# Performance work log

Measured on AMD Instinct MI355X. Metric: run time of the kernel, lower is better.

Reference implementation:

```python
import jax, jax.numpy as jnp
import numpy as np

NEG_SLOPE = 0.01  # nn.LeakyReLU default


def setup_inputs() -> dict:
    key = jax.random.key(0)
    ks = jax.random.split(key, 13)
    B, T, C = 128, 2048, 16
    CO = 8 * C          # 128 conv out channels == LSTM input
    H = 128             # LSTM hidden
    G = 4 * H           # gate dim
    OUT = 1
    s = 0.08            # keep recurrence stable over 2048 steps
    f32 = jnp.float32
    return {
        "x": jax.random.normal(ks[0], (B, T, C), f32),
        "conv_w": jax.random.normal(ks[1], (CO, C, 3), f32) * s,
        "conv_b": jax.random.normal(ks[2], (CO,), f32) * s,
        "w_ih0": jax.random.normal(ks[3], (G, CO), f32) * s,
        "w_hh0": jax.random.normal(ks[4], (G, H), f32) * s,
        "b_ih0": jax.random.normal(ks[5], (G,), f32) * s,
        "b_hh0": jax.random.normal(ks[6], (G,), f32) * s,
        "w_ih1": jax.random.normal(ks[7], (G, H), f32) * s,
        "w_hh1": jax.random.normal(ks[8], (G, H), f32) * s,
        "b_ih1": jax.random.normal(ks[9], (G,), f32) * s,
        "b_hh1": jax.random.normal(ks[10], (G,), f32) * s,
        "lin_w": jax.random.normal(ks[11], (OUT, H), f32) * s,
        "lin_b": jax.random.normal(ks[12], (OUT,), f32) * s,
    }


def _lstm_cell(gates, c):
    i, f, g, o = jnp.split(gates, 4, axis=-1)  # torch gate order i,f,g,o
    c_new = jax.nn.sigmoid(f) * c + jax.nn.sigmoid(i) * jnp.tanh(g)
    h_new = jax.nn.sigmoid(o) * jnp.tanh(c_new)
    return h_new, c_new


def reference(x, conv_w, conv_b, w_ih0, w_hh0, b_ih0, b_hh0,
              w_ih1, w_hh1, b_ih1, b_hh1, lin_w, lin_b):
    B, T, C = x.shape
    H = w_hh0.shape[1]
    # Conv1d k=3 pad=1 over time: [B,C,T] -> [B,8C,T]
    xc = jnp.transpose(x, (0, 2, 1))
    y = jax.lax.conv_general_dilated(
        xc, conv_w, window_strides=(1,), padding=((1, 1),),
        dimension_numbers=("NCH", "OIH", "NCH"))
    y = y + conv_b[None, :, None]
    y = jnp.where(y >= 0, y, NEG_SLOPE * y)  # LeakyReLU
    seq = jnp.transpose(y, (0, 2, 1))  # [B,T,8C]
    # Precompute layer-0 input projection (biases folded in, constant per step)
    x0 = jnp.einsum("btc,gc->btg", seq, w_ih0) + (b_ih0 + b_hh0)  # [B,T,4H]
    b1 = b_ih1 + b_hh1

    def step(carry, xt):
        h0, c0, h1, c1 = carry
        h0, c0 = _lstm_cell(xt + h0 @ w_hh0.T, c0)
        h1, c1 = _lstm_cell(h0 @ w_ih1.T + b1 + h1 @ w_hh1.T, c1)
        return (h0, c0, h1, c1), h1

    zeros = jnp.zeros((B, H), x.dtype)
    init = (zeros, zeros, zeros, zeros)
    xs = jnp.transpose(x0, (1, 0, 2))  # [T,B,4H]
    _, hs = jax.lax.scan(step, init, xs)  # [T,B,H]
    pooled = hs.mean(axis=0)  # adaptive_avg_pool1d(.,1) == mean over time
    return pooled @ lin_w.T + lin_b
```

## Files before the change

kernel.cpp:

```cpp
#include <hip/hip_runtime.h>
#include <hip/hip_fp16.h>
#include <cstdint>
#include <cstddef>

#define B_ 128
#define T_ 2048
#define C_ 16
#define CO_ 128
#define H_ 128
#define G_ 512
#define WCV 184
#define NBLK (72 + WCV)
#define L2E  1.4426950408889634f
#define L2E2 2.8853900817779268f

typedef _Float16 half8 __attribute__((ext_vector_type(8)));
typedef float f32x4 __attribute__((ext_vector_type(4)));

__device__ __forceinline__ unsigned packh2f(float a, float b) {
  union { _Float16 h[2]; unsigned u; } x;
  x.h[0] = (_Float16)a; x.h[1] = (_Float16)b;
  return x.u;
}

__device__ __forceinline__ float rcpf(float x) { return __builtin_amdgcn_rcpf(x); }

__device__ __forceinline__ float exp2f_(float x) {
#if __has_builtin(__builtin_amdgcn_exp2f)
  return __builtin_amdgcn_exp2f(x);
#else
  return __expf(x * 0.6931471805599453f);
#endif
}

__device__ __forceinline__ void block_sync() {
  asm volatile("s_waitcnt lgkmcnt(0)" ::: "memory");
  __builtin_amdgcn_s_barrier();
  asm volatile("" ::: "memory");
}

__device__ __forceinline__ int ld_rlx(const int* p) {
  return __hip_atomic_load(p, __ATOMIC_RELAXED, __HIP_MEMORY_SCOPE_AGENT);
}
__device__ __forceinline__ void st_rlx(int* p, int v) {
  __hip_atomic_store(p, v, __ATOMIC_RELAXED, __HIP_MEMORY_SCOPE_AGENT);
}

__device__ __forceinline__ float lstm_cell1(float iv, float fv, float gv,
                                            float ov, float& c) {
  gv = fminf(fmaxf(gv, -43.3f), 43.3f);
  float ei = exp2f_(-iv), ef = exp2f_(-fv), eg = exp2f_(gv);
  float P = (1.f + ei) * (eg + 1.f);
  float Q = 1.f + ef;
  float num = c * P + (eg - 1.f) * Q;
  float cN = num * rcpf(Q * P);
  c = cN;
  float cc = fminf(fmaxf(cN, -15.f), 15.f);
  float eo = exp2f_(-ov), ec = exp2f_(L2E2 * cc);
  return (ec - 1.f) * rcpf((1.f + eo) * (ec + 1.f));
}

__global__ __launch_bounds__(256) void pack_kernel(
    const float* __restrict__ w_ih0, const float* __restrict__ w_hh0,
    const float* __restrict__ w_ih1, const float* __restrict__ w_hh1,
    const float* __restrict__ b_ih1, const float* __restrict__ b_hh1,
    uint4* __restrict__ Wf0, uint4* __restrict__ Wih1f,
    uint4* __restrict__ Whh1f, uint4* __restrict__ WB0f,
    f32x4* __restrict__ b1fD) {
  int tid = blockIdx.x * 256 + threadIdx.x;
  if (tid < 24576) {
    int u = tid & 8191, L = u & 63, s = (u >> 6) & 3, tl = (u >> 8) & 3, w = u >> 10;
    int which = tid >> 13;
    const float* src = (which == 0) ? w_hh0 : (which == 1) ? w_ih1 : w_hh1;
    uint4* dst = (which == 0) ? Wf0 : (which == 1) ? Wih1f : Whh1f;
    int m = (w + 8 * tl) * 16 + (L & 15);
    float sc = (tl == 2) ? L2E2 : L2E;
    int k0 = s * 32 + (L >> 4) * 8;
    const float* p = src + m * 128 + k0;
    uint4 o;
    o.x = packh2f(p[0] * sc, p[1] * sc); o.y = packh2f(p[2] * sc, p[3] * sc);
    o.z = packh2f(p[4] * sc, p[5] * sc); o.w = packh2f(p[6] * sc, p[7] * sc);
    dst[u] = o;
  } else if (tid < 32768) {
    int u = tid - 24576, L = u & 63, s = (u >> 6) & 3, nt = u >> 8;
    int g = nt * 16 + (L & 15);
    float sc = ((nt >> 3) == 2) ? L2E2 : L2E;
    int k0 = s * 32 + (L >> 4) * 8;
    const float* p = w_ih0 + g * 128 + k0;
    uint4 o;
    o.x = packh2f(p[0] * sc, p[1] * sc); o.y = packh2f(p[2] * sc, p[3] * sc);
    o.z = packh2f(p[4] * sc, p[5] * sc); o.w = packh2f(p[6] * sc, p[7] * sc);
    WB0f[u] = o;
  } else if (tid < 34816) {
    int u2 = tid - 32768;
    int tl = u2 & 3, L = (u2 >> 2) & 63, w = u2 >> 8;
    int q = L >> 4;
    float sc = (tl == 2) ? L2E2 : L2E;
    f32x4 o;
#pragma unroll
    for (int reg = 0; reg < 4; ++reg) {
      int row = (w + 8 * tl) * 16 + q * 4 + reg;
      o[reg] = (b_ih1[row] + b_hh1[row]) * sc;
    }
    b1fD[u2] = o;
  }
}

__global__ __launch_bounds__(512, 1) void persist_kernel(
    const float* __restrict__ x, const float* __restrict__ conv_w,
    const float* __restrict__ conv_b, const float* __restrict__ b_ih0,
    const float* __restrict__ b_hh0,
    const uint4* __restrict__ Wf0, const uint4* __restrict__ Wih1f,
    const uint4* __restrict__ Whh1f, const uint4* __restrict__ WB0f,
    const f32x4* __restrict__ b1fD,
    uint4* __restrict__ x0f, uint2* __restrict__ h0g, uint4* __restrict__ z1f,
    float* __restrict__ psave, int* __restrict__ flags,
    int rmask, int rmask2) {
  __shared__ __align__(16) union {
    struct { float xs[34 * 16]; _Float16 yh[32 * 136]; _Float16 x0S[32 * 512]; } wk;
    struct { _Float16 h[2][16 * 136]; } rc;
    struct { _Float16 h4[2][576]; } rc4;
  } sm;

  int* xready = flags;
  int* l0p = flags + 2048;
  int* l0c = flags + 2560;
  int* z1p = flags + 3072;
  int* l1p = flags + 3200;

  const int bid = blockIdx.x;
  const int tid = threadIdx.x;
  const int w = tid >> 6, L = tid & 63, q = L >> 4, n = L & 15;

  if (bid < 32 || (bid >= 40 && bid < 72)) {
    const bool isL0 = bid < 32;
    const int rb = isL0 ? bid : bid - 40;
    const int grp = (rb & 7) * 4 + (rb >> 3);
    half8 WA[4][4];
    {
      const uint4* Wsrc = isL0 ? Wf0 : Whh1f;
#pragma unroll
      for (int tl = 0; tl < 4; ++tl)
#pragma unroll
        for (int s = 0; s < 4; ++s)
          WA[tl][s] = __builtin_bit_cast(half8, Wsrc[((w * 4 + tl) * 4 + s) * 64 + L]);
    }
    float cst = 0.f, pool = 0.f;
    for (int idx = tid; idx < 576; idx += 512) ((unsigned*)sm.rc4.h4)[idx] = 0u;
    __syncthreads();

    const int n4 = n & 3;
    const int n16 = (grp & 3) * 4 + n4;
    const int uc = w * 16 + (L >> 2);
    const int bc = L & 3;
    const int rsel = (L >> 2) & 3;
    const bool sb0 = (rsel & 1) != 0, sb1 = (rsel & 2) != 0;

    const uint4* rp = (isL0 ? x0f : z1f) +
        (((size_t)(grp >> 2) * 8 + w) * 64 + (q * 16 + n16)) * 2;
    const int rmk = isL0 ? rmask : rmask2;
    uint2* hgp = h0g + (((grp >> 2) * 16 + ((grp & 3) * 4 + (tid & 3))) * 32 + (tid >> 2));
    uint4 pa[4], pb[4];

    for (int g = 0; g < 64; ++g) {
      const int p0g = g * 32;
      if (tid == 0) {
        if (isL0) {
          while (ld_rlx(&xready[g * 32 + grp]) < 4) __builtin_amdgcn_s_sleep(2);
          if (g < 63)
            while (ld_rlx(&xready[(g + 1) * 32 + grp]) < 4) __builtin_amdgcn_s_sleep(2);
        } else {
          int tgt = p0g + 40; if (tgt > T_) tgt = T_;
          while (ld_rlx(&z1p[(grp >> 2) * 16]) < tgt) __builtin_amdgcn_s_sleep(1);
        }
        __builtin_amdgcn_fence(__ATOMIC_ACQUIRE, "agent");
      }
      block_sync();
      if (g == 0) {
#pragma unroll
        for (int k = 0; k < 4; ++k) {
          pa[k] = rp[(size_t)k * 8192];
          pb[k] = rp[(size_t)k * 8192 + 1];
        }
      }
#pragma unroll 1
      for (int io = 0; io < 8; ++io) {
#pragma unroll
        for (int k = 0; k < 4; ++k) {
          const int t = p0g + io * 4 + k;
          const int c = t & 1, p = c ^ 1;
          f32x4 acc[4];
          {
            half8 xlo = __builtin_bit_cast(half8, pa[k]);
            half8 xhi = __builtin_bit_cast(half8, pb[k]);
            acc[0] = (f32x4){(float)xlo[0], (float)xlo[1], (float)xlo[2], (float)xlo[3]};
            acc[1] = (f32x4){(float)xlo[4], (float)xlo[5], (float)xlo[6], (float)xlo[7]};
            acc[2] = (f32x4){(float)xhi[0], (float)xhi[1], (float)xhi[2], (float)xhi[3]};
            acc[3] = (f32x4){(float)xhi[4], (float)xhi[5], (float)xhi[6], (float)xhi[7]};
          }
          half8 B0[4];
#pragma unroll
          for (int s = 0; s < 4; ++s)
            B0[s] = *(const half8*)&sm.rc4.h4[p][n4 * 144 + s * 32 + q * 8];
#pragma unroll
          for (int s = 0; s < 4; ++s)
#pragma unroll
            for (int tl = 0; tl < 4; ++tl)
              acc[tl] = __builtin_amdgcn_mfma_f32_16x16x32_f16(WA[tl][s], B0[s], acc[tl], 0, 0, 0);

          {
            int tn = t + 4; if (tn > T_ - 1) tn = T_ - 1;
            const size_t so = (size_t)(tn & rmk) * 8192;
            pa[k] = rp[so];
            pb[k] = rp[so + 1];
          }

          float gi, gf, gg, go;
          {
            float lo, hi;
            lo = sb0 ? acc[0][1] : acc[0][0]; hi = sb0 ? acc[0][3] : acc[0][2];
            gi = sb1 ? hi : lo;
            lo = sb0 ? acc[1][1] : acc[1][0]; hi = sb0 ? acc[1][3] : acc[1][2];
            gf = sb1 ? hi : lo;
            lo = sb0 ? acc[2][1] : acc[2][0]; hi = sb0 ? acc[2][3] : acc[2][2];
            gg = sb1 ? hi : lo;
            lo = sb0 ? acc[3][1] : acc[3][0]; hi = sb0 ? acc[3][3] : acc[3][2];
            go = sb1 ? hi : lo;
          }
          float hv = lstm_cell1(gi, gf, gg, go, cst);
          if (!isL0) pool += hv;
          sm.rc4.h4[c][bc * 144 + uc] = (_Float16)hv;

          block_sync();
          if (isL0) {
            if (k == 3) {
              asm volatile("s_waitcnt vmcnt(8)" ::: "memory");
              if (tid == 0) st_rlx(&l0p[grp * 16], t - 3);
            }
            if (tid < 128)
              hgp[(size_t)t * 4096] =
                  *(const uint2*)&sm.rc4.h4[c][(tid & 3) * 144 + (tid >> 2) * 4];
          }
        }
      }
      if (tid == 0) {
        if (isL0) st_rlx(&l0c[grp * 16], p0g + 32);
        else if (g & 1) st_rlx(&l1p[grp * 16], p0g + 32);
      }
    }
    if (isL0) {
      asm volatile("s_waitcnt vmcnt(0)" ::: "memory");
      __builtin_amdgcn_s_barrier();
      if (tid == 0)
        __hip_atomic_store(&l0p[grp * 16], T_, __ATOMIC_RELEASE,
                           __HIP_MEMORY_SCOPE_AGENT);
    } else {
      psave[(size_t)(grp * 4 + bc) * 128 + uc] = pool;
    }
  } else if (bid < 40) {
    const int b16 = bid - 32;
    half8 WI[4][4];
#pragma unroll
    for (int tl = 0; tl < 4; ++tl)
#pragma unroll
      for (int s = 0; s < 4; ++s)
        WI[tl][s] = __builtin_bit_cast(half8, Wih1f[((w * 4 + tl) * 4 + s) * 64 + L]);
    f32x4 b1v[4];
#pragma unroll
    for (int tl = 0; tl < 4; ++tl) b1v[tl] = b1fD[(w * 64 + L) * 4 + tl];

    const int n2 = tid >> 5, jq = tid & 31;
    const uint2* hsrc = h0g + ((b16 * 16 + n2) * 32 + jq);
    uint4* zdst = z1f + (((size_t)b16 * 8 + w) * 64 + L) * 2;
    const int R2 = rmask2 + 1;
    uint2 hpf[4];

#pragma unroll 1
    for (int p0 = 0; p0 < T_; p0 += 4) {
      if (tid < 4) {
        const int gj = b16 * 4 + tid;
        while (ld_rlx(&l0p[gj * 16]) < p0 + 4) __builtin_amdgcn_s_sleep(1);
        __builtin_amdgcn_fence(__ATOMIC_ACQUIRE, "agent");
      } else if (tid >= 4 && tid < 8 && p0 + 4 > R2) {
        const int gj = b16 * 4 + (tid - 4);
        const int need = p0 + 12 - R2;
        while (ld_rlx(&l1p[gj * 16]) < need) __builtin_amdgcn_s_sleep(8);
      }
      block_sync();
#pragma unroll
      for (int k = 0; k < 4; ++k) hpf[k] = hsrc[(size_t)(p0 + k) * 4096];
#pragma unroll
      for (int k = 0; k < 4; ++k) {
        const int t = p0 + k;
        const int c = t & 1;
        *(uint2*)&sm.rc.h[c][n2 * 136 + jq * 4] = hpf[k];
        block_sync();
        half8 B[4];
#pragma unroll
        for (int s = 0; s < 4; ++s)
          B[s] = *(const half8*)&sm.rc.h[c][n * 136 + s * 32 + q * 8];
        f32x4 acc[4];
#pragma unroll
        for (int tl = 0; tl < 4; ++tl) acc[tl] = b1v[tl];
#pragma unroll
        for (int s = 0; s < 4; ++s)
#pragma unroll
          for (int tl = 0; tl < 4; ++tl)
            acc[tl] = __builtin_amdgcn_mfma_f32_16x16x32_f16(WI[tl][s], B[s], acc[tl], 0, 0, 0);
        uint4 o0, o1;
        o0.x = packh2f(acc[0][0], acc[0][1]); o0.y = packh2f(acc[0][2], acc[0][3]);
        o0.z = packh2f(acc[1][0], acc[1][1]); o0.w = packh2f(acc[1][2], acc[1][3]);
        o1.x = packh2f(acc[2][0], acc[2][1]); o1.y = packh2f(acc[2][2], acc[2][3]);
        o1.z = packh2f(acc[3][0], acc[3][1]); o1.w = packh2f(acc[3][2], acc[3][3]);
        const size_t zs = (size_t)(t & rmask2) * 8192;
        zdst[zs] = o0;
        zdst[zs + 1] = o1;
      }
      asm volatile("s_waitcnt vmcnt(12)" ::: "memory");
      block_sync();
      if (tid == 0) st_rlx(&z1p[b16 * 16], p0);
    }
    asm volatile("s_waitcnt vmcnt(0)" ::: "memory");
    __builtin_amdgcn_s_barrier();
    if (tid == 0)
      __hip_atomic_store(&z1p[b16 * 16], T_, __ATOMIC_RELEASE,
                         __HIP_MEMORY_SCOPE_AGENT);
  } else {
    const int wi = bid - 72;
    const int co = tid & 127;
    float cw[48];
#pragma unroll
    for (int i = 0; i < 12; ++i) {
      const float4 v = *(const float4*)(conv_w + co * 48 + i * 4);
      cw[i * 4 + 0] = v.x; cw[i * 4 + 1] = v.y;
      cw[i * 4 + 2] = v.z; cw[i * 4 + 3] = v.w;
    }
    const float cb = conv_b[co];
    half8 WB[4][4];
#pragma unroll
    for (int nt4 = 0; nt4 < 4; ++nt4)
#pragma unroll
      for (int s = 0; s < 4; ++s)
        WB[nt4][s] = __builtin_bit_cast(half8, WB0f[((w * 4 + nt4) * 4 + s) * 64 + L]);
    float b0v[4];
#pragma unroll
    for (int nt4 = 0; nt4 < 4; ++nt4) {
      int gg = (w * 4 + nt4) * 16 + n;
      b0v[nt4] = (b_ih0[gg] + b_hh0[gg]) * (((gg >> 7) == 2) ? L2E2 : L2E);
    }
    const int R = rmask + 1;

    for (int u = wi; u < 8192; u += WCV) {
      const int tile = u >> 7, b = u & 127;
      const int t0c = tile * 32;
      if (t0c + 40 > R) {
        const int need = t0c + 40 - R;
        if (tid == 0)
          while (ld_rlx(&l0c[(b >> 2) * 16]) < need)
            __builtin_amdgcn_s_sleep(8);
      }
      __syncthreads();

      for (int idx = tid; idx < 544; idx += 512) {
        int row = idx >> 4, cc2 = idx & 15;
        int gt = t0c - 1 + row;
        sm.wk.xs[idx] = (gt >= 0 && gt < T_) ? x[((size_t)b * T_ + gt) * C_ + cc2] : 0.f;
      }
      __syncthreads();

#pragma unroll
      for (int pp = 0; pp < 8; ++pp) {
        int r = pp * 4 + (tid >> 7);
        float acc = cb;
#pragma unroll
        for (int c16 = 0; c16 < 16; ++c16)
#pragma unroll
          for (int kk = 0; kk < 3; ++kk)
            acc += sm.wk.xs[(r + kk) * 16 + c16] * cw[c16 * 3 + kk];
        acc = acc >= 0.f ? acc : 0.01f * acc;
        sm.wk.yh[r * 136 + co] = (_Float16)acc;
      }
      __syncthreads();

#pragma unroll
      for (int mt = 0; mt < 2; ++mt) {
        half8 A[4];
#pragma unroll
        for (int s = 0; s < 4; ++s)
          A[s] = *(const half8*)&sm.wk.yh[(mt * 16 + n) * 136 + s * 32 + q * 8];
#pragma unroll
        for (int nt4 = 0; nt4 < 4; ++nt4) {
          f32x4 acc = {b0v[nt4], b0v[nt4], b0v[nt4], b0v[nt4]};
#pragma unroll
          for (int s = 0; s < 4; ++s)
            acc = __builtin_amdgcn_mfma_f32_16x16x32_f16(A[s], WB[nt4][s], acc, 0, 0, 0);
          int tau = w * 4 + nt4;
          int off = (tau & 7) * 64 + (n >> 2) * 16 + (tau >> 3) * 4 + (n & 3);
#pragma unroll
          for (int reg = 0; reg < 4; ++reg)
            sm.wk.x0S[(mt * 16 + q * 4 + reg) * 512 + off] = (_Float16)acc[reg];
        }
      }
      __syncthreads();

      const int bn = b & 15, bb16 = b >> 4;
      const int trb = t0c & rmask;
#pragma unroll
      for (int kk = 0; kk < 2; ++kk) {
        int cc = kk * 512 + tid;
        int r = cc >> 5, wq = cc & 31;
        int w2 = wq >> 2, q2 = wq & 3;
        const uint4* src = (const uint4*)&sm.wk.x0S[r * 512 + wq * 16];
        size_t gidx = ((((size_t)(trb + r) * 8 + bb16) * 8 + w2) * 64 + (bn + 16 * q2)) * 2;
        x0f[gidx] = src[0];
        x0f[gidx + 1] = src[1];
      }
      asm volatile("s_waitcnt vmcnt(0)" ::: "memory");
      __syncthreads();
      if (tid == 0)
        __hip_atomic_fetch_add(&xready[tile * 32 + (b >> 2)], 1, __ATOMIC_RELEASE,
                               __HIP_MEMORY_SCOPE_AGENT);
    }
  }
}

__global__ __launch_bounds__(128) void final_kernel(
    const float* __restrict__ psave, const float* __restrict__ lin_w,
    const float* __restrict__ lin_b, float* __restrict__ out) {
  int b = threadIdx.x;
  float acc = 0.f;
  const f32x4* pv = (const f32x4*)(psave + (size_t)b * 128);
  const f32x4* lw = (const f32x4*)lin_w;
#pragma unroll
  for (int u = 0; u < 32; ++u) {
    f32x4 v = pv[u], l = lw[u];
    acc += v[0] * l[0] + v[1] * l[1] + v[2] * l[2] + v[3] * l[3];
  }
  out[b] = acc * (1.0f / (float)T_) + lin_b[0];
}

extern "C" void kernel_launch(void* const* d_in, const int* in_sizes, int n_in,
                              void* d_out, int out_size, void* d_ws, size_t ws_size,
                              hipStream_t stream) {
  (void)in_sizes; (void)n_in; (void)out_size;
  const float* x      = (const float*)d_in[0];
  const float* conv_w = (const float*)d_in[1];
  const float* conv_b = (const float*)d_in[2];
  const float* w_ih0  = (const float*)d_in[3];
  const float* w_hh0  = (const float*)d_in[4];
  const float* b_ih0  = (const float*)d_in[5];
  const float* b_hh0  = (const float*)d_in[6];
  const float* w_ih1  = (const float*)d_in[7];
  const float* w_hh1  = (const float*)d_in[8];
  const float* b_ih1  = (const float*)d_in[9];
  const float* b_hh1  = (const float*)d_in[10];
  const float* lin_w  = (const float*)d_in[11];
  const float* lin_b  = (const float*)d_in[12];

  char* ws = (char*)d_ws;
  uint4* Wf0   = (uint4*)(ws + 0);
  uint4* Wih1f = (uint4*)(ws + 131072);
  uint4* Whh1f = (uint4*)(ws + 262144);
  uint4* WB0f  = (uint4*)(ws + 393216);
  f32x4* b1fD  = (f32x4*)(ws + 524288);
  float* psave = (float*)(ws + 557056);
  int*   flags = (int*)(ws + 622592);
  uint2* h0g   = (uint2*)(ws + 638976);
  const size_t base = 638976 + 67108864;

  int R = 256, R2 = 256;
  while (R > 64 && base + ((size_t)R + (size_t)R2) * 131072 > ws_size) {
    R >>= 1; R2 >>= 1;
  }
  uint4* x0f = (uint4*)(ws + base);
  uint4* z1f = (uint4*)(ws + base + (size_t)R * 131072);

  hipMemsetAsync(flags, 0, 16384, stream);
  pack_kernel<<<136, 256, 0, stream>>>(w_ih0, w_hh0, w_ih1, w_hh1, b_ih1, b_hh1,
                                       Wf0, Wih1f, Whh1f, WB0f, b1fD);
  persist_kernel<<<NBLK, 512, 0, stream>>>(
      x, conv_w, conv_b, b_ih0, b_hh0, Wf0, Wih1f, Whh1f, WB0f, b1fD,
      x0f, h0g, z1f, psave, flags, R - 1, R2 - 1);
  final_kernel<<<1, 128, 0, stream>>>(psave, lin_w, lin_b, (float*)d_out);
}
```

Before: 1.643 ms.

## Fuse layer-1 input projection into layer-1 recurrent blocks, drop z1 stage

Removes the 8 dedicated blocks that computed the layer-1 input projection (h0 @ W_ih1 + b1) into a global z1 ring buffer. Each layer-1 recurrent block now reads h0 from global into shared memory with a short prefetch and does both the W_ih1 and W_hh1 MFMAs per step. The conv/projection blocks grow from 184 to 192 to use the freed slots. This cuts a pipeline stage, its flags and its global round-trips, but doubles the MFMA work and register weight footprint on the layer-1 critical path.

Measured after the change: 1.637 ms. Within noise of the previous version (-0.3%).

```diff
diff --git a/kernel.cpp b/kernel.cpp
--- a/kernel.cpp
+++ b/kernel.cpp
@@ -9,8 +9,8 @@
 #define CO_ 128
 #define H_ 128
 #define G_ 512
-#define WCV 184
-#define NBLK (72 + WCV)
+#define WCV 192
+#define NBLK (64 + WCV)
 #define L2E  1.4426950408889634f
 #define L2E2 2.8853900817779268f
 
@@ -113,40 +113,31 @@
     const uint4* __restrict__ Wf0, const uint4* __restrict__ Wih1f,
     const uint4* __restrict__ Whh1f, const uint4* __restrict__ WB0f,
     const f32x4* __restrict__ b1fD,
-    uint4* __restrict__ x0f, uint2* __restrict__ h0g, uint4* __restrict__ z1f,
-    float* __restrict__ psave, int* __restrict__ flags,
-    int rmask, int rmask2) {
+    uint4* __restrict__ x0f, uint2* __restrict__ h0g,
+    float* __restrict__ psave, int* __restrict__ flags, int rmask) {
   __shared__ __align__(16) union {
     struct { float xs[34 * 16]; _Float16 yh[32 * 136]; _Float16 x0S[32 * 512]; } wk;
-    struct { _Float16 h[2][16 * 136]; } rc;
-    struct { _Float16 h4[2][576]; } rc4;
+    struct { _Float16 hb[2][576]; _Float16 h0b[2][576]; } rc4;
   } sm;
 
   int* xready = flags;
-  int* l0p = flags + 2048;
-  int* l0c = flags + 2560;
-  int* z1p = flags + 3072;
-  int* l1p = flags + 3200;
+  int* l0c = flags + 2048;
+  int* l0p = flags + 2560;
 
   const int bid = blockIdx.x;
   const int tid = threadIdx.x;
   const int w = tid >> 6, L = tid & 63, q = L >> 4, n = L & 15;
 
-  if (bid < 32 || (bid >= 40 && bid < 72)) {
-    const bool isL0 = bid < 32;
-    const int rb = isL0 ? bid : bid - 40;
-    const int grp = (rb & 7) * 4 + (rb >> 3);
+  if (bid < 32) {
+    const int grp = (bid & 7) * 4 + (bid >> 3);
     half8 WA[4][4];
-    {
-      const uint4* Wsrc = isL0 ? Wf0 : Whh1f;
-#pragma unroll
-      for (int tl = 0; tl < 4; ++tl)
-#pragma unroll
-        for (int s = 0; s < 4; ++s)
-          WA[tl][s] = __builtin_bit_cast(half8, Wsrc[((w * 4 + tl) * 4 + s) * 64 + L]);
-    }
-    float cst = 0.f, pool = 0.f;
-    for (int idx = tid; idx < 576; idx += 512) ((unsigned*)sm.rc4.h4)[idx] = 0u;
+#pragma unroll
+    for (int tl = 0; tl < 4; ++tl)
+#pragma unroll
+      for (int s = 0; s < 4; ++s)
+        WA[tl][s] = __builtin_bit_cast(half8, Wf0[((w * 4 + tl) * 4 + s) * 64 + L]);
+    float cst = 0.f;
+    for (int idx = tid; idx < 576; idx += 512) ((unsigned*)sm.rc4.hb)[idx] = 0u;
     __syncthreads();
 
     const int n4 = n & 3;
@@ -156,23 +147,16 @@
     const int rsel = (L >> 2) & 3;
     const bool sb0 = (rsel & 1) != 0, sb1 = (rsel & 2) != 0;
 
-    const uint4* rp = (isL0 ? x0f : z1f) +
-        (((size_t)(grp >> 2) * 8 + w) * 64 + (q * 16 + n16)) * 2;
-    const int rmk = isL0 ? rmask : rmask2;
+    const uint4* rp = x0f + (((size_t)(grp >> 2) * 8 + w) * 64 + (q * 16 + n16)) * 2;
     uint2* hgp = h0g + (((grp >> 2) * 16 + ((grp & 3) * 4 + (tid & 3))) * 32 + (tid >> 2));
     uint4 pa[4], pb[4];
 
     for (int g = 0; g < 64; ++g) {
       const int p0g = g * 32;
       if (tid == 0) {
-        if (isL0) {
-          while (ld_rlx(&xready[g * 32 + grp]) < 4) __builtin_amdgcn_s_sleep(2);
-          if (g < 63)
-            while (ld_rlx(&xready[(g + 1) * 32 + grp]) < 4) __builtin_amdgcn_s_sleep(2);
-        } else {
-          int tgt = p0g + 40; if (tgt > T_) tgt = T_;
-          while (ld_rlx(&z1p[(grp >> 2) * 16]) < tgt) __builtin_amdgcn_s_sleep(1);
-        }
+        while (ld_rlx(&xready[g * 32 + grp]) < 4) __builtin_amdgcn_s_sleep(2);
+        if (g < 63)
+          while (ld_rlx(&xready[(g + 1) * 32 + grp]) < 4) __builtin_amdgcn_s_sleep(2);
         __builtin_amdgcn_fence(__ATOMIC_ACQUIRE, "agent");
       }
       block_sync();
@@ -201,7 +185,7 @@
           half8 B0[4];
 #pragma unroll
           for (int s = 0; s < 4; ++s)
-            B0[s] = *(const half8*)&sm.rc4.h4[p][n4 * 144 + s * 32 + q * 8];
+            B0[s] = *(const half8*)&sm.rc4.hb[p][n4 * 144 + s * 32 + q * 8];
 #pragma unroll
           for (int s = 0; s < 4; ++s)
 #pragma unroll
@@ -210,7 +194,7 @@
 
           {
             int tn = t + 4; if (tn > T_ - 1) tn = T_ - 1;
-            const size_t so = (size_t)(tn & rmk) * 8192;
+            const size_t so = (size_t)(tn & rmask) * 8192;
             pa[k] = rp[so];
             pb[k] = rp[so + 1];
           }
@@ -228,105 +212,129 @@
             go = sb1 ? hi : lo;
           }
           float hv = lstm_cell1(gi, gf, gg, go, cst);
-          if (!isL0) pool += hv;
-          sm.rc4.h4[c][bc * 144 + uc] = (_Float16)hv;
+          sm.rc4.hb[c][bc * 144 + uc] = (_Float16)hv;
 
           block_sync();
-          if (isL0) {
-            if (k == 3) {
-              asm volatile("s_waitcnt vmcnt(8)" ::: "memory");
-              if (tid == 0) st_rlx(&l0p[grp * 16], t - 3);
-            }
-            if (tid < 128)
-              hgp[(size_t)t * 4096] =
-                  *(const uint2*)&sm.rc4.h4[c][(tid & 3) * 144 + (tid >> 2) * 4];
-          }
+          if (k == 3) {
+            asm volatile("s_waitcnt vmcnt(8)" ::: "memory");
+            if (tid == 0) st_rlx(&l0p[grp * 16], t - 3);
+          }
+          if (tid < 128)
+            hgp[(size_t)t * 4096] =
+                *(const uint2*)&sm.rc4.hb[c][(tid & 3) * 144 + (tid >> 2) * 4];
         }
       }
-      if (tid == 0) {
-        if (isL0) st_rlx(&l0c[grp * 16], p0g + 32);
-        else if (g & 1) st_rlx(&l1p[grp * 16], p0g + 32);
-      }
-    }
-    if (isL0) {
-      asm volatile("s_waitcnt vmcnt(0)" ::: "memory");
-      __builtin_amdgcn_s_barrier();
-      if (tid == 0)
-        __hip_atomic_store(&l0p[grp * 16], T_, __ATOMIC_RELEASE,
-                           __HIP_MEMORY_SCOPE_AGENT);
-    } else {
-      psave[(size_t)(grp * 4 + bc) * 128 + uc] = pool;
-    }
-  } else if (bid < 40) {
-    const int b16 = bid - 32;
-    half8 WI[4][4];
-#pragma unroll
-    for (int tl = 0; tl < 4; ++tl)
-#pragma unroll
-      for (int s = 0; s < 4; ++s)
-        WI[tl][s] = __builtin_bit_cast(half8, Wih1f[((w * 4 + tl) * 4 + s) * 64 + L]);
-    f32x4 b1v[4];
-#pragma unroll
-    for (int tl = 0; tl < 4; ++tl) b1v[tl] = b1fD[(w * 64 + L) * 4 + tl];
-
-    const int n2 = tid >> 5, jq = tid & 31;
-    const uint2* hsrc = h0g + ((b16 * 16 + n2) * 32 + jq);
-    uint4* zdst = z1f + (((size_t)b16 * 8 + w) * 64 + L) * 2;
-    const int R2 = rmask2 + 1;
-    uint2 hpf[4];
-
-#pragma unroll 1
-    for (int p0 = 0; p0 < T_; p0 += 4) {
-      if (tid < 4) {
-        const int gj = b16 * 4 + tid;
-        while (ld_rlx(&l0p[gj * 16]) < p0 + 4) __builtin_amdgcn_s_sleep(1);
-        __builtin_amdgcn_fence(__ATOMIC_ACQUIRE, "agent");
-      } else if (tid >= 4 && tid < 8 && p0 + 4 > R2) {
-        const int gj = b16 * 4 + (tid - 4);
-        const int need = p0 + 12 - R2;
-        while (ld_rlx(&l1p[gj * 16]) < need) __builtin_amdgcn_s_sleep(8);
-      }
-      block_sync();
-#pragma unroll
-      for (int k = 0; k < 4; ++k) hpf[k] = hsrc[(size_t)(p0 + k) * 4096];
-#pragma unroll
-      for (int k = 0; k < 4; ++k) {
-        const int t = p0 + k;
-        const int c = t & 1;
-        *(uint2*)&sm.rc.h[c][n2 * 136 + jq * 4] = hpf[k];
-        block_sync();
-        half8 B[4];
-#pragma unroll
-        for (int s = 0; s < 4; ++s)
-          B[s] = *(const half8*)&sm.rc.h[c][n * 136 + s * 32 + q * 8];
-        f32x4 acc[4];
-#pragma unroll
-        for (int tl = 0; tl < 4; ++tl) acc[tl] = b1v[tl];
-#pragma unroll
-        for (int s = 0; s < 4; ++s)
-#pragma unroll
-          for (int tl = 0; tl < 4; ++tl)
-            acc[tl] = __builtin_amdgcn_mfma_f32_16x16x32_f16(WI[tl][s], B[s], acc[tl], 0, 0, 0);
-        uint4 o0, o1;
-        o0.x = packh2f(acc[0][0], acc[0][1]); o0.y = packh2f(acc[0][2], acc[0][3]);
-        o0.z = packh2f(acc[1][0], acc[1][1]); o0.w = packh2f(acc[1][2], acc[1][3]);
-        o1.x = packh2f(acc[2][0], acc[2][1]); o1.y = packh2f(acc[2][2], acc[2][3]);
-        o1.z = packh2f(acc[3][0], acc[3][1]); o1.w = packh2f(acc[3][2], acc[3][3]);
-        const size_t zs = (size_t)(t & rmask2) * 8192;
-        zdst[zs] = o0;
-        zdst[zs + 1] = o1;
-      }
-      asm volatile("s_waitcnt vmcnt(12)" ::: "memory");
-      block_sync();
-      if (tid == 0) st_rlx(&z1p[b16 * 16], p0);
+      if (tid == 0) st_rlx(&l0c[grp * 16], p0g + 32);
     }
     asm volatile("s_waitcnt vmcnt(0)" ::: "memory");
     __builtin_amdgcn_s_barrier();
     if (tid == 0)
-      __hip_atomic_store(&z1p[b16 * 16], T_, __ATOMIC_RELEASE,
+      __hip_atomic_store(&l0p[grp * 16], T_, __ATOMIC_RELEASE,
                          __HIP_MEMORY_SCOPE_AGENT);
+  } else if (bid < 64) {
+    const int rb = bid - 32;
+    const int grp = (rb & 7) * 4 + (rb >> 3);
+    half8 WA[4][4], WI[4][4];
+#pragma unroll
+    for (int tl = 0; tl < 4; ++tl)
+#pragma unroll
+      for (int s = 0; s < 4; ++s) {
+        WA[tl][s] = __builtin_bit_cast(half8, Whh1f[((w * 4 + tl) * 4 + s) * 64 + L]);
+        WI[tl][s] = __builtin_bit_cast(half8, Wih1f[((w * 4 + tl) * 4 + s) * 64 + L]);
+      }
+    f32x4 b1v[4];
+#pragma unroll
+    for (int tl = 0; tl < 4; ++tl) b1v[tl] = b1fD[(w * 64 + L) * 4 + tl];
+
+    float cst = 0.f, pool = 0.f;
+    for (int idx = tid; idx < 1152; idx += 512) ((unsigned*)&sm.rc4)[idx] = 0u;
+    __syncthreads();
+
+    const int n4 = n & 3;
+    const int uc = w * 16 + (L >> 2);
+    const int bc = L & 3;
+    const int rsel = (L >> 2) & 3;
+    const bool sb0 = (rsel & 1) != 0, sb1 = (rsel & 2) != 0;
+
+    const uint2* hgp = h0g + (((size_t)(grp >> 2) * 16 + ((grp & 3) * 4 + (tid & 3))) * 32 + (tid >> 2));
+    const int h0off = (tid & 3) * 144 + (tid >> 2) * 4;
+    uint2 pf[4];
+
+    if (tid == 0) {
+      while (ld_rlx(&l0p[grp * 16]) < 8) __builtin_amdgcn_s_sleep(1);
+      __builtin_amdgcn_fence(__ATOMIC_ACQUIRE, "agent");
+    }
+    block_sync();
+    if (tid < 128) {
+      uint2 h00 = hgp[0];
+      *(uint2*)&sm.rc4.h0b[0][h0off] = h00;
+#pragma unroll
+      for (int k = 0; k < 4; ++k) pf[k] = hgp[(size_t)(k + 1) * 4096];
+    }
+    block_sync();
+
+#pragma unroll 1
+    for (int g = 0; g < 64; ++g) {
+      const int p0g = g * 32;
+      if (tid == 0) {
+        int tgt = p0g + 40; if (tgt > T_) tgt = T_;
+        while (ld_rlx(&l0p[grp * 16]) < tgt) __builtin_amdgcn_s_sleep(1);
+        __builtin_amdgcn_fence(__ATOMIC_ACQUIRE, "agent");
+      }
+      block_sync();
+#pragma unroll 1
+      for (int io = 0; io < 8; ++io) {
+#pragma unroll
+        for (int k = 0; k < 4; ++k) {
+          const int t = p0g + io * 4 + k;
+          const int c = t & 1, p = c ^ 1;
+          half8 B1[4], B0h[4];
+#pragma unroll
+          for (int s = 0; s < 4; ++s) {
+            B1[s] = *(const half8*)&sm.rc4.hb[p][n4 * 144 + s * 32 + q * 8];
+            B0h[s] = *(const half8*)&sm.rc4.h0b[c][n4 * 144 + s * 32 + q * 8];
+          }
+          if (tid < 128) {
+            *(uint2*)&sm.rc4.h0b[p][h0off] = pf[k];
+            int tn = t + 5; if (tn > T_ - 1) tn = T_ - 1;
+            pf[k] = hgp[(size_t)tn * 4096];
+          }
+          f32x4 acc[4];
+#pragma unroll
+          for (int tl = 0; tl < 4; ++tl) acc[tl] = b1v[tl];
+#pragma unroll
+          for (int s = 0; s < 4; ++s)
+#pragma unroll
+            for (int tl = 0; tl < 4; ++tl)
+              acc[tl] = __builtin_amdgcn_mfma_f32_16x16x32_f16(WI[tl][s], B0h[s], acc[tl], 0, 0, 0);
+#pragma unroll
+          for (int s = 0; s < 4; ++s)
+#pragma unroll
+            for (int tl = 0; tl < 4; ++tl)
+              acc[tl] = __builtin_amdgcn_mfma_f32_16x16x32_f16(WA[tl][s], B1[s], acc[tl], 0, 0, 0);
+
+          float gi, gf, gg, go;
+          {
+            float lo, hi;
+            lo = sb0 ? acc[0][1] : acc[0][0]; hi = sb0 ? acc[0][3] : acc[0][2];
+            gi = sb1 ? hi : lo;
+            lo = sb0 ? acc[1][1] : acc[1][0]; hi = sb0 ? acc[1][3] : acc[1][2];
+            gf = sb1 ? hi : lo;
+            lo = sb0 ? acc[2][1] : acc[2][0]; hi = sb0 ? acc[2][3] : acc[2][2];
+            gg = sb1 ? hi : lo;
+            lo = sb0 ? acc[3][1] : acc[3][0]; hi = sb0 ? acc[3][3] : acc[3][2];
+            go = sb1 ? hi : lo;
+          }
+          float hv = lstm_cell1(gi, gf, gg, go, cst);
+          pool += hv;
+          sm.rc4.hb[c][bc * 144 + uc] = (_Float16)hv;
+          block_sync();
+        }
+      }
+    }
+    psave[(size_t)(grp * 4 + bc) * 128 + uc] = pool;
   } else {
-    const int wi = bid - 72;
+    const int wi = bid - 64;
     const int co = tid & 127;
     float cw[48];
 #pragma unroll
@@ -468,18 +476,15 @@
   uint2* h0g   = (uint2*)(ws + 638976);
   const size_t base = 638976 + 67108864;
 
-  int R = 256, R2 = 256;
-  while (R > 64 && base + ((size_t)R + (size_t)R2) * 131072 > ws_size) {
-    R >>= 1; R2 >>= 1;
-  }
+  int R = 256;
+  while (R > 64 && base + (size_t)R * 131072 > ws_size) R >>= 1;
   uint4* x0f = (uint4*)(ws + base);
-  uint4* z1f = (uint4*)(ws + base + (size_t)R * 131072);
 
   hipMemsetAsync(flags, 0, 16384, stream);
   pack_kernel<<<136, 256, 0, stream>>>(w_ih0, w_hh0, w_ih1, w_hh1, b_ih1, b_hh1,
                                        Wf0, Wih1f, Whh1f, WB0f, b1fD);
   persist_kernel<<<NBLK, 512, 0, stream>>>(
       x, conv_w, conv_b, b_ih0, b_hh0, Wf0, Wih1f, Whh1f, WB0f, b1fD,
-      x0f, h0g, z1f, psave, flags, R - 1, R2 - 1);
+      x0f, h0g, psave, flags, R - 1);
   final_kernel<<<1, 128, 0, stream>>>(psave, lin_w, lin_b, (float*)d_out);
 }
```

## Merge layer-0 and layer-1 recurrence blocks into skewed single blocks

Applied to the files above, without the earlier changes.

The separate layer-0 and layer-1 recurrent block sets are merged, so each of 32 blocks now runs both recurrences. Layer 1 trails layer 0 by a fixed lag of 56 steps and shares the per-step barrier, with a tail loop that finishes the last lagged steps. This frees 32 blocks, which go to the conv/input-projection workers (WCV 184 to 216). The cost is more work per step on the critical serial path, more registers for both weight sets, and tighter coupling to the z1 producer through the lag.

Measured after the change: 2.308 ms. 1.4x slower.

```diff
diff --git a/kernel.cpp b/kernel.cpp
--- a/kernel.cpp
+++ b/kernel.cpp
@@ -9,8 +9,9 @@
 #define CO_ 128
 #define H_ 128
 #define G_ 512
-#define WCV 184
-#define NBLK (72 + WCV)
+#define LAG 56
+#define WCV 216
+#define NBLK (40 + WCV)
 #define L2E  1.4426950408889634f
 #define L2E2 2.8853900817779268f
 
@@ -58,6 +59,12 @@
   float cc = fminf(fmaxf(cN, -15.f), 15.f);
   float eo = exp2f_(-ov), ec = exp2f_(L2E2 * cc);
   return (ec - 1.f) * rcpf((1.f + eo) * (ec + 1.f));
+}
+
+__device__ __forceinline__ float sel4(const f32x4 v, bool sb0, bool sb1) {
+  float lo = sb0 ? v[1] : v[0];
+  float hi = sb0 ? v[3] : v[2];
+  return sb1 ? hi : lo;
 }
 
 __global__ __launch_bounds__(256) void pack_kernel(
@@ -119,7 +126,7 @@
   __shared__ __align__(16) union {
     struct { float xs[34 * 16]; _Float16 yh[32 * 136]; _Float16 x0S[32 * 512]; } wk;
     struct { _Float16 h[2][16 * 136]; } rc;
-    struct { _Float16 h4[2][576]; } rc4;
+    struct { _Float16 h0b[2][576]; _Float16 h1b[2][576]; } rcm;
   } sm;
 
   int* xready = flags;
@@ -132,23 +139,8 @@
   const int tid = threadIdx.x;
   const int w = tid >> 6, L = tid & 63, q = L >> 4, n = L & 15;
 
-  if (bid < 32 || (bid >= 40 && bid < 72)) {
-    const bool isL0 = bid < 32;
-    const int rb = isL0 ? bid : bid - 40;
-    const int grp = (rb & 7) * 4 + (rb >> 3);
-    half8 WA[4][4];
-    {
-      const uint4* Wsrc = isL0 ? Wf0 : Whh1f;
-#pragma unroll
-      for (int tl = 0; tl < 4; ++tl)
-#pragma unroll
-        for (int s = 0; s < 4; ++s)
-          WA[tl][s] = __builtin_bit_cast(half8, Wsrc[((w * 4 + tl) * 4 + s) * 64 + L]);
-    }
-    float cst = 0.f, pool = 0.f;
-    for (int idx = tid; idx < 576; idx += 512) ((unsigned*)sm.rc4.h4)[idx] = 0u;
-    __syncthreads();
-
+  if (bid < 32) {
+    const int grp = (bid & 7) * 4 + (bid >> 3);
     const int n4 = n & 3;
     const int n16 = (grp & 3) * 4 + n4;
     const int uc = w * 16 + (L >> 2);
@@ -156,107 +148,171 @@
     const int rsel = (L >> 2) & 3;
     const bool sb0 = (rsel & 1) != 0, sb1 = (rsel & 2) != 0;
 
-    const uint4* rp = (isL0 ? x0f : z1f) +
-        (((size_t)(grp >> 2) * 8 + w) * 64 + (q * 16 + n16)) * 2;
-    const int rmk = isL0 ? rmask : rmask2;
+    half8 WA0[4][4], WA1[4][4];
+#pragma unroll
+    for (int tl = 0; tl < 4; ++tl)
+#pragma unroll
+      for (int s = 0; s < 4; ++s) {
+        WA0[tl][s] = __builtin_bit_cast(half8, Wf0[((w * 4 + tl) * 4 + s) * 64 + L]);
+        WA1[tl][s] = __builtin_bit_cast(half8, Whh1f[((w * 4 + tl) * 4 + s) * 64 + L]);
+      }
+
+    float c0 = 0.f, c1 = 0.f, pool = 0.f;
+    for (int idx = tid; idx < 1152; idx += 512) ((unsigned*)&sm.rcm)[idx] = 0u;
+    __syncthreads();
+
+    const uint4* rp = x0f + (((size_t)(grp >> 2) * 8 + w) * 64 + (q * 16 + n16)) * 2;
+    const uint4* zp = z1f + (((size_t)(grp >> 2) * 8 + w) * 64 + (q * 16 + n16)) * 2;
     uint2* hgp = h0g + (((grp >> 2) * 16 + ((grp & 3) * 4 + (tid & 3))) * 32 + (tid >> 2));
-    uint4 pa[4], pb[4];
+    uint4 pa, pb, za, zb;
 
     for (int g = 0; g < 64; ++g) {
       const int p0g = g * 32;
       if (tid == 0) {
-        if (isL0) {
-          while (ld_rlx(&xready[g * 32 + grp]) < 4) __builtin_amdgcn_s_sleep(2);
-          if (g < 63)
-            while (ld_rlx(&xready[(g + 1) * 32 + grp]) < 4) __builtin_amdgcn_s_sleep(2);
-        } else {
-          int tgt = p0g + 40; if (tgt > T_) tgt = T_;
-          while (ld_rlx(&z1p[(grp >> 2) * 16]) < tgt) __builtin_amdgcn_s_sleep(1);
-        }
+        while (ld_rlx(&xready[g * 32 + grp]) < 4) __builtin_amdgcn_s_sleep(2);
+        if (g < 63)
+          while (ld_rlx(&xready[(g + 1) * 32 + grp]) < 4) __builtin_amdgcn_s_sleep(2);
+        const int zt = p0g - 16;
+        if (zt > 0)
+          while (ld_rlx(&z1p[(grp >> 2) * 16]) < zt) __builtin_amdgcn_s_sleep(1);
         __builtin_amdgcn_fence(__ATOMIC_ACQUIRE, "agent");
       }
       block_sync();
-      if (g == 0) {
-#pragma unroll
-        for (int k = 0; k < 4; ++k) {
-          pa[k] = rp[(size_t)k * 8192];
-          pb[k] = rp[(size_t)k * 8192 + 1];
-        }
-      }
+      if (g == 0) { pa = rp[0]; pb = rp[1]; }
+      if (g == 1) { za = zp[0]; zb = zp[1]; }
 #pragma unroll 1
       for (int io = 0; io < 8; ++io) {
 #pragma unroll
         for (int k = 0; k < 4; ++k) {
           const int t = p0g + io * 4 + k;
-          const int c = t & 1, p = c ^ 1;
-          f32x4 acc[4];
+          const int u = t - LAG;
+          const int ct = t & 1, pt = ct ^ 1;
+
           {
-            half8 xlo = __builtin_bit_cast(half8, pa[k]);
-            half8 xhi = __builtin_bit_cast(half8, pb[k]);
-            acc[0] = (f32x4){(float)xlo[0], (float)xlo[1], (float)xlo[2], (float)xlo[3]};
-            acc[1] = (f32x4){(float)xlo[4], (float)xlo[5], (float)xlo[6], (float)xlo[7]};
-            acc[2] = (f32x4){(float)xhi[0], (float)xhi[1], (float)xhi[2], (float)xhi[3]};
-            acc[3] = (f32x4){(float)xhi[4], (float)xhi[5], (float)xhi[6], (float)xhi[7]};
+            half8 B0[4];
+#pragma unroll
+            for (int s = 0; s < 4; ++s)
+              B0[s] = *(const half8*)&sm.rcm.h0b[pt][n4 * 144 + s * 32 + q * 8];
+            f32x4 acc[4];
+            {
+              half8 xlo = __builtin_bit_cast(half8, pa);
+              half8 xhi = __builtin_bit_cast(half8, pb);
+              acc[0] = (f32x4){(float)xlo[0], (float)xlo[1], (float)xlo[2], (float)xlo[3]};
+              acc[1] = (f32x4){(float)xlo[4], (float)xlo[5], (float)xlo[6], (float)xlo[7]};
+              acc[2] = (f32x4){(float)xhi[0], (float)xhi[1], (float)xhi[2], (float)xhi[3]};
+              acc[3] = (f32x4){(float)xhi[4], (float)xhi[5], (float)xhi[6], (float)xhi[7]};
+            }
+            {
+              int tn = t + 1; if (tn > T_ - 1) tn = T_ - 1;
+              const size_t so = (size_t)(tn & rmask) * 8192;
+              pa = rp[so];
+              pb = rp[so + 1];
+            }
+#pragma unroll
+            for (int s = 0; s < 4; ++s)
+#pragma unroll
+              for (int tl = 0; tl < 4; ++tl)
+                acc[tl] = __builtin_amdgcn_mfma_f32_16x16x32_f16(WA0[tl][s], B0[s], acc[tl], 0, 0, 0);
+            float gi = sel4(acc[0], sb0, sb1);
+            float gf = sel4(acc[1], sb0, sb1);
+            float gg = sel4(acc[2], sb0, sb1);
+            float go = sel4(acc[3], sb0, sb1);
+            float hv = lstm_cell1(gi, gf, gg, go, c0);
+            sm.rcm.h0b[ct][bc * 144 + uc] = (_Float16)hv;
           }
-          half8 B0[4];
-#pragma unroll
-          for (int s = 0; s < 4; ++s)
-            B0[s] = *(const half8*)&sm.rc4.h4[p][n4 * 144 + s * 32 + q * 8];
-#pragma unroll
-          for (int s = 0; s < 4; ++s)
-#pragma unroll
-            for (int tl = 0; tl < 4; ++tl)
-              acc[tl] = __builtin_amdgcn_mfma_f32_16x16x32_f16(WA[tl][s], B0[s], acc[tl], 0, 0, 0);
-
-          {
-            int tn = t + 4; if (tn > T_ - 1) tn = T_ - 1;
-            const size_t so = (size_t)(tn & rmk) * 8192;
-            pa[k] = rp[so];
-            pb[k] = rp[so + 1];
+
+          if (u >= 0) {
+            half8 B1[4];
+#pragma unroll
+            for (int s = 0; s < 4; ++s)
+              B1[s] = *(const half8*)&sm.rcm.h1b[pt][n4 * 144 + s * 32 + q * 8];
+            f32x4 acc[4];
+            {
+              half8 xlo = __builtin_bit_cast(half8, za);
+              half8 xhi = __builtin_bit_cast(half8, zb);
+              acc[0] = (f32x4){(float)xlo[0], (float)xlo[1], (float)xlo[2], (float)xlo[3]};
+              acc[1] = (f32x4){(float)xlo[4], (float)xlo[5], (float)xlo[6], (float)xlo[7]};
+              acc[2] = (f32x4){(float)xhi[0], (float)xhi[1], (float)xhi[2], (float)xhi[3]};
+              acc[3] = (f32x4){(float)xhi[4], (float)xhi[5], (float)xhi[6], (float)xhi[7]};
+            }
+            {
+              const size_t so = (size_t)((u + 1) & rmask2) * 8192;
+              za = zp[so];
+              zb = zp[so + 1];
+            }
+#pragma unroll
+            for (int s = 0; s < 4; ++s)
+#pragma unroll
+              for (int tl = 0; tl < 4; ++tl)
+                acc[tl] = __builtin_amdgcn_mfma_f32_16x16x32_f16(WA1[tl][s], B1[s], acc[tl], 0, 0, 0);
+            float gi = sel4(acc[0], sb0, sb1);
+            float gf = sel4(acc[1], sb0, sb1);
+            float gg = sel4(acc[2], sb0, sb1);
+            float go = sel4(acc[3], sb0, sb1);
+            float hv = lstm_cell1(gi, gf, gg, go, c1);
+            pool += hv;
+            sm.rcm.h1b[ct][bc * 144 + uc] = (_Float16)hv;
           }
 
-          float gi, gf, gg, go;
-          {
-            float lo, hi;
-            lo = sb0 ? acc[0][1] : acc[0][0]; hi = sb0 ? acc[0][3] : acc[0][2];
-            gi = sb1 ? hi : lo;
-            lo = sb0 ? acc[1][1] : acc[1][0]; hi = sb0 ? acc[1][3] : acc[1][2];
-            gf = sb1 ? hi : lo;
-            lo = sb0 ? acc[2][1] : acc[2][0]; hi = sb0 ? acc[2][3] : acc[2][2];
-            gg = sb1 ? hi : lo;
-            lo = sb0 ? acc[3][1] : acc[3][0]; hi = sb0 ? acc[3][3] : acc[3][2];
-            go = sb1 ? hi : lo;
+          block_sync();
+          if (k == 3) {
+            asm volatile("s_waitcnt vmcnt(12)" ::: "memory");
+            if (tid == 0) st_rlx(&l0p[grp * 16], t - 3);
           }
-          float hv = lstm_cell1(gi, gf, gg, go, cst);
-          if (!isL0) pool += hv;
-          sm.rc4.h4[c][bc * 144 + uc] = (_Float16)hv;
-
-          block_sync();
-          if (isL0) {
-            if (k == 3) {
-              asm volatile("s_waitcnt vmcnt(8)" ::: "memory");
-              if (tid == 0) st_rlx(&l0p[grp * 16], t - 3);
-            }
-            if (tid < 128)
-              hgp[(size_t)t * 4096] =
-                  *(const uint2*)&sm.rc4.h4[c][(tid & 3) * 144 + (tid >> 2) * 4];
-          }
+          if (tid < 128)
+            hgp[(size_t)t * 4096] =
+                *(const uint2*)&sm.rcm.h0b[ct][(tid & 3) * 144 + (tid >> 2) * 4];
         }
       }
       if (tid == 0) {
-        if (isL0) st_rlx(&l0c[grp * 16], p0g + 32);
-        else if (g & 1) st_rlx(&l1p[grp * 16], p0g + 32);
-      }
-    }
-    if (isL0) {
-      asm volatile("s_waitcnt vmcnt(0)" ::: "memory");
-      __builtin_amdgcn_s_barrier();
-      if (tid == 0)
-        __hip_atomic_store(&l0p[grp * 16], T_, __ATOMIC_RELEASE,
-                           __HIP_MEMORY_SCOPE_AGENT);
-    } else {
-      psave[(size_t)(grp * 4 + bc) * 128 + uc] = pool;
-    }
+        st_rlx(&l0c[grp * 16], p0g + 32);
+        const int lp = p0g - 24;
+        if (lp > 0) st_rlx(&l1p[grp * 16], lp);
+      }
+    }
+    asm volatile("s_waitcnt vmcnt(0)" ::: "memory");
+    __builtin_amdgcn_s_barrier();
+    if (tid == 0)
+      __hip_atomic_store(&l0p[grp * 16], T_, __ATOMIC_RELEASE,
+                         __HIP_MEMORY_SCOPE_AGENT);
+#pragma unroll 1
+    for (int u = T_ - LAG; u < T_; ++u) {
+      if (tid == 0) {
+        while (ld_rlx(&z1p[(grp >> 2) * 16]) < u + 1) __builtin_amdgcn_s_sleep(1);
+        __builtin_amdgcn_fence(__ATOMIC_ACQUIRE, "agent");
+      }
+      block_sync();
+      const int cu = u & 1, pu = cu ^ 1;
+      half8 B1[4];
+#pragma unroll
+      for (int s = 0; s < 4; ++s)
+        B1[s] = *(const half8*)&sm.rcm.h1b[pu][n4 * 144 + s * 32 + q * 8];
+      const size_t zs = (size_t)(u & rmask2) * 8192;
+      uint4 za2 = zp[zs], zb2 = zp[zs + 1];
+      f32x4 acc[4];
+      {
+        half8 xlo = __builtin_bit_cast(half8, za2);
+        half8 xhi = __builtin_bit_cast(half8, zb2);
+        acc[0] = (f32x4){(float)xlo[0], (float)xlo[1], (float)xlo[2], (float)xlo[3]};
+        acc[1] = (f32x4){(float)xlo[4], (float)xlo[5], (float)xlo[6], (float)xlo[7]};
+        acc[2] = (f32x4){(float)xhi[0], (float)xhi[1], (float)xhi[2], (float)xhi[3]};
+        acc[3] = (f32x4){(float)xhi[4], (float)xhi[5], (float)xhi[6], (float)xhi[7]};
+      }
+#pragma unroll
+      for (int s = 0; s < 4; ++s)
+#pragma unroll
+        for (int tl = 0; tl < 4; ++tl)
+          acc[tl] = __builtin_amdgcn_mfma_f32_16x16x32_f16(WA1[tl][s], B1[s], acc[tl], 0, 0, 0);
+      float gi = sel4(acc[0], sb0, sb1);
+      float gf = sel4(acc[1], sb0, sb1);
+      float gg = sel4(acc[2], sb0, sb1);
+      float go = sel4(acc[3], sb0, sb1);
+      float hv = lstm_cell1(gi, gf, gg, go, c1);
+      pool += hv;
+      sm.rcm.h1b[cu][bc * 144 + uc] = (_Float16)hv;
+      block_sync();
+    }
+    psave[(size_t)(grp * 4 + bc) * 128 + uc] = pool;
   } else if (bid < 40) {
     const int b16 = bid - 32;
     half8 WI[4][4];
@@ -326,7 +382,7 @@
       __hip_atomic_store(&z1p[b16 * 16], T_, __ATOMIC_RELEASE,
                          __HIP_MEMORY_SCOPE_AGENT);
   } else {
-    const int wi = bid - 72;
+    const int wi = bid - 40;
     const int co = tid & 127;
     float cw[48];
 #pragma unroll
@@ -425,11 +481,11 @@
 }
 
 __global__ __launch_bounds__(128) void final_kernel(
-    const float* __restrict__ psave, const float* __restrict__ lin_w,
+    const f32x4* __restrict__ psave_, const float* __restrict__ lin_w,
     const float* __restrict__ lin_b, float* __restrict__ out) {
   int b = threadIdx.x;
   float acc = 0.f;
-  const f32x4* pv = (const f32x4*)(psave + (size_t)b * 128);
+  const f32x4* pv = (const f32x4*)((const float*)psave_ + (size_t)b * 128);
   const f32x4* lw = (const f32x4*)lin_w;
 #pragma unroll
   for (int u = 0; u < 32; ++u) {
@@ -481,5 +537,6 @@
   persist_kernel<<<NBLK, 512, 0, stream>>>(
       x, conv_w, conv_b, b_ih0, b_hh0, Wf0, Wih1f, Whh1f, WB0f, b1fD,
       x0f, h0g, z1f, psave, flags, R - 1, R2 - 1);
-  final_kernel<<<1, 128, 0, stream>>>(psave, lin_w, lin_b, (float*)d_out);
-}
+  final_kernel<<<1, 128, 0, stream>>>((const f32x4*)psave, lin_w, lin_b,
+                                      (float*)d_out);
+}
```
